# Optimization experiments

Measured on AMD Instinct MI355X. Metric: run time of the kernel, lower is better.

The kernel has to match this reference:

```python
import jax, jax.numpy as jnp
import numpy as np

D = 1024
H = 16
K = 32768
EPS = 1e-5


def setup_inputs() -> dict:
    key = jax.random.key(0)
    ks = jax.random.split(key, 12)
    s = 1.0 / np.sqrt(D)
    return {
        "query": jax.random.normal(ks[0], (D,), jnp.float32),
        "neighbors": jax.random.normal(ks[1], (K, D), jnp.float32),
        # nn.MultiheadAttention params
        "in_proj_w": jax.random.uniform(ks[2], (3 * D, D), jnp.float32, -s, s),
        "in_proj_b": jnp.zeros((3 * D,), jnp.float32),
        "out_proj_w": jax.random.uniform(ks[3], (D, D), jnp.float32, -s, s),
        "out_proj_b": jnp.zeros((D,), jnp.float32),
        # FFN params
        "w1": jax.random.uniform(ks[4], (4 * D, D), jnp.float32, -s, s),
        "b1": jnp.zeros((4 * D,), jnp.float32),
        "w2": jax.random.uniform(ks[5], (D, 4 * D), jnp.float32, -s, s),
        "b2": jnp.zeros((D,), jnp.float32),
        # LayerNorm params
        "g1": jnp.ones((D,), jnp.float32),
        "be1": jnp.zeros((D,), jnp.float32),
        "g2": jnp.ones((D,), jnp.float32),
        "be2": jnp.zeros((D,), jnp.float32),
    }


def _layernorm(x, g, b):
    m = jnp.mean(x, axis=-1, keepdims=True)
    v = jnp.var(x, axis=-1, keepdims=True)
    return (x - m) * jax.lax.rsqrt(v + EPS) * g + b


def reference(query, neighbors, in_proj_w, in_proj_b, out_proj_w, out_proj_b,
              w1, b1, w2, b2, g1, be1, g2, be2):
    dh = D // H
    wq, wk, wv = in_proj_w[:D], in_proj_w[D:2 * D], in_proj_w[2 * D:]
    bq, bk, bv = in_proj_b[:D], in_proj_b[D:2 * D], in_proj_b[2 * D:]

    q = (query @ wq.T + bq).reshape(H, dh)            # [H, dh]
    k = (neighbors @ wk.T + bk).reshape(K, H, dh)     # [K, H, dh]
    v = (neighbors @ wv.T + bv).reshape(K, H, dh)

    scores = jnp.einsum('hd,khd->hk', q, k) / np.sqrt(dh)  # [H, K]
    attn = jax.nn.softmax(scores, axis=-1)
    ctx = jnp.einsum('hk,khd->hd', attn, v).reshape(D)      # [D]
    attn_out = ctx @ out_proj_w.T + out_proj_b

    x = _layernorm(query + attn_out, g1, be1)
    ffn = jax.nn.gelu(x @ w1.T + b1, approximate=False) @ w2.T + b2
    return _layernorm(x + ffn, g2, be2)
```

## Files before the change

### kernel.cpp

```cpp
#include <hip/hip_runtime.h>
#include <hip/hip_bf16.h>

#define D 1024
#define H 16
#define DH 64
#define KN 32768
#define EPS 1e-5f

__device__ __forceinline__ float wave_sum(float v){
  #pragma unroll
  for (int off = 32; off; off >>= 1) v += __shfl_xor(v, off, 64);
  return v;
}

#define GLL(gp, lp) __builtin_amdgcn_global_load_lds((const __attribute__((address_space(1))) void*)(gp), (__attribute__((address_space(3))) void*)(lp), 16, 0, 0)

__global__ void g_qproj(const float* __restrict__ query, const float* __restrict__ ipw,
                        const float* __restrict__ ipb, float* __restrict__ q){
  int j = blockIdx.x, l = threadIdx.x;
  const float4* qv = (const float4*)(query + l*16);
  const float4* wv = (const float4*)(ipw + (size_t)j*D + l*16);
  float acc = 0.f;
  #pragma unroll
  for (int t = 0; t < 4; t++){
    float4 a = qv[t], b = wv[t];
    acc += a.x*b.x + a.y*b.y + a.z*b.z + a.w*b.w;
  }
  acc = wave_sum(acc);
  if (l == 0) q[j] = acc + ipb[j];
}

__global__ __launch_bounds__(256) void g_qk(const float* __restrict__ ipw, const float* __restrict__ ipb,
                                            const float* __restrict__ q, float* __restrict__ qk,
                                            float* __restrict__ sb){
  int b = blockIdx.x, t = threadIdx.x;
  int h = b >> 2, sl = b & 3;
  int jg = t >> 6, c = t & 63;
  __shared__ float qh[DH];
  __shared__ float4 red[256];
  if (t < DH) qh[t] = q[h*DH + t];
  __syncthreads();
  if (t < DH){
    float p = qh[t] * ipb[D + h*DH + t];
    p = wave_sum(p);
    if (t == 0 && sl == 0) sb[h] = p;
  }
  float4 acc = make_float4(0.f,0.f,0.f,0.f);
  for (int jj = 0; jj < 16; jj++){
    int j = jg*16 + jj;
    float4 w = *((const float4*)(ipw + (size_t)(D + h*DH + j)*D) + sl*64 + c);
    float qj = qh[j];
    acc.x += qj*w.x; acc.y += qj*w.y; acc.z += qj*w.z; acc.w += qj*w.w;
  }
  red[t] = acc;
  __syncthreads();
  if (jg == 0){
    float4 a = red[c], b1 = red[64+c], c1 = red[128+c], d1 = red[192+c];
    float4 r = make_float4(a.x+b1.x+c1.x+d1.x, a.y+b1.y+c1.y+d1.y,
                           a.z+b1.z+c1.z+d1.z, a.w+b1.w+c1.w+d1.w);
    ((float4*)(qk + h*D))[sl*64 + c] = r;
  }
}

__global__ void g_attn(const float* __restrict__ nbr, const float* __restrict__ qk,
                       const float* __restrict__ sb, float* __restrict__ lpart,
                       float* __restrict__ part, int rows_per_blk){
  __shared__ __align__(16) float tile[2][8*D];
  int t = threadIdx.x;
  int h = t >> 6, ci = t & 63;
  int wb = t & ~63;
  float sbh = sb[h];

  float qkv[16];
  {
    const float4* qp = (const float4*)(qk + h*D);
    #pragma unroll
    for (int c = 0; c < 4; c++){
      float4 f = qp[c*64 + ci];
      qkv[4*c]=f.x; qkv[4*c+1]=f.y; qkv[4*c+2]=f.z; qkv[4*c+3]=f.w;
    }
  }
  float acc[16];
  #pragma unroll
  for (int i = 0; i < 16; i++) acc[i] = 0.f;
  float lsum = 0.f;

  const int k0 = blockIdx.x * rows_per_blk;
  const int ntiles = rows_per_blk >> 3;
  const uint4* gb = (const uint4*)nbr;

  {
    const uint4* g = gb + (size_t)k0*256;
    #pragma unroll
    for (int i = 0; i < 2; i++) GLL(g + i*1024 + t, &tile[0][(i*1024 + wb)*4]);
  }
  __syncthreads();

  #pragma unroll 1
  for (int tl = 0; tl < ntiles; tl++){
    int cur = tl & 1;
    if (tl + 1 < ntiles){
      const uint4* g = gb + (size_t)(k0 + (tl+1)*8)*256;
      #pragma unroll
      for (int i = 0; i < 2; i++) GLL(g + i*1024 + t, &tile[cur^1][(i*1024 + wb)*4]);
    }
    #pragma unroll 1
    for (int r = 0; r < 8; r++){
      const float4* row4 = (const float4*)(tile[cur]) + r*256;
      float xf[16];
      float s = 0.f;
      #pragma unroll
      for (int c = 0; c < 4; c++){
        float4 a = row4[c*64 + ci];
        xf[4*c]=a.x; xf[4*c+1]=a.y; xf[4*c+2]=a.z; xf[4*c+3]=a.w;
        s += a.x*qkv[4*c] + a.y*qkv[4*c+1] + a.z*qkv[4*c+2] + a.w*qkv[4*c+3];
      }
      s = wave_sum(s);
      float p = __expf((s + sbh)*0.125f);
      lsum += p;
      #pragma unroll
      for (int i = 0; i < 16; i++) acc[i] += p*xf[i];
    }
    __syncthreads();
  }

  if (ci == 0) lpart[blockIdx.x*H + h] = lsum;
  float4* o = (float4*)(part + (size_t)blockIdx.x*(H*D) + h*D);
  #pragma unroll
  for (int c = 0; c < 4; c++)
    o[c*64 + ci] = make_float4(acc[4*c], acc[4*c+1], acc[4*c+2], acc[4*c+3]);
}

__global__ __launch_bounds__(256) void g_red(const float* __restrict__ part, const float* __restrict__ lpart,
                                             float* __restrict__ nb, float* __restrict__ lh, int nblk){
  int b = blockIdx.x, t = threadIdx.x;
  if (b == 64){
    if (t < H){
      float s = 0.f;
      for (int c = 0; c < nblk; c++) s += lpart[c*H + t];
      lh[t] = s;
    }
    return;
  }
  int o = b*256 + t;
  float s = 0.f;
  #pragma unroll 8
  for (int c = 0; c < nblk; c++) s += part[(size_t)c*(H*D) + o];
  nb[o] = s;
}

__global__ void g_ctx(const float* __restrict__ ipw, const float* __restrict__ ipb,
                      const float* __restrict__ nb, const float* __restrict__ lh,
                      float* __restrict__ ctx){
  int j = blockIdx.x, l = threadIdx.x, h = j >> 6;
  const float4* wv = (const float4*)(ipw + (size_t)(2*D + j)*D + l*16);
  const float4* nv = (const float4*)(nb + h*D + l*16);
  float acc = 0.f;
  #pragma unroll
  for (int t = 0; t < 4; t++){
    float4 b = wv[t], n = nv[t];
    acc += b.x*n.x + b.y*n.y + b.z*n.z + b.w*n.w;
  }
  acc = wave_sum(acc);
  if (l == 0) ctx[j] = acc/lh[h] + ipb[2*D + j];
}

__global__ void g_attnout(const float* __restrict__ opw, const float* __restrict__ opb,
                          const float* __restrict__ query, const float* __restrict__ ctx,
                          float* __restrict__ xb){
  int j = blockIdx.x, l = threadIdx.x;
  const float4* wv = (const float4*)(opw + (size_t)j*D + l*16);
  const float4* cv = (const float4*)(ctx + l*16);
  float acc = 0.f;
  #pragma unroll
  for (int t = 0; t < 4; t++){
    float4 b = wv[t], c = cv[t];
    acc += b.x*c.x + b.y*c.y + b.z*c.z + b.w*c.w;
  }
  acc = wave_sum(acc);
  if (l == 0) xb[j] = query[j] + acc + opb[j];
}

__global__ __launch_bounds__(256) void g_ffn1(const float* __restrict__ w1, const float* __restrict__ b1,
                                              const float* __restrict__ xb,
                                              const float* __restrict__ g1, const float* __restrict__ be1,
                                              float* __restrict__ xln, float* __restrict__ h1){
  int t = threadIdx.x, b = blockIdx.x;
  __shared__ float xs[D];
  __shared__ float red[8];
  float4 v = ((const float4*)xb)[t];
  float s = wave_sum(v.x + v.y + v.z + v.w);
  if ((t & 63) == 0) red[t >> 6] = s;
  __syncthreads();
  float m = (red[0]+red[1]+red[2]+red[3]) * (1.0f/D);
  float4 d = make_float4(v.x-m, v.y-m, v.z-m, v.w-m);
  float s2 = wave_sum(d.x*d.x + d.y*d.y + d.z*d.z + d.w*d.w);
  if ((t & 63) == 0) red[4 + (t >> 6)] = s2;
  __syncthreads();
  float var = (red[4]+red[5]+red[6]+red[7]) * (1.0f/D);
  float rs = rsqrtf(var + EPS);
  float4 gg = ((const float4*)g1)[t], bb = ((const float4*)be1)[t];
  float4 r = make_float4(d.x*rs*gg.x + bb.x, d.y*rs*gg.y + bb.y,
                         d.z*rs*gg.z + bb.z, d.w*rs*gg.w + bb.w);
  ((float4*)xs)[t] = r;
  if (b == 0) ((float4*)xln)[t] = r;
  __syncthreads();

  int w = t >> 6, l = t & 63;
  const float4* xs4 = (const float4*)xs;
  #pragma unroll 1
  for (int rr = 0; rr < 4; rr++){
    int j = b*16 + w*4 + rr;
    const float4* wr = (const float4*)(w1 + (size_t)j*D);
    float a = 0.f;
    #pragma unroll
    for (int c = 0; c < 4; c++){
      float4 ww = wr[c*64 + l], xx = xs4[c*64 + l];
      a += ww.x*xx.x + ww.y*xx.y + ww.z*xx.z + ww.w*xx.w;
    }
    a = wave_sum(a);
    if (l == 0){
      float z = a + b1[j];
      h1[j] = 0.5f*z*(1.0f + erff(z*0.70710678118654752f));
    }
  }
}

__global__ void g_ffn2(const float* __restrict__ w2, const float* __restrict__ b2v,
                       const float* __restrict__ h1, float* __restrict__ y){
  int j = blockIdx.x, l = threadIdx.x;
  const float4* wv = (const float4*)(w2 + (size_t)j*4096 + l*64);
  const float4* hv = (const float4*)(h1 + l*64);
  float acc = 0.f;
  #pragma unroll
  for (int t = 0; t < 16; t++){
    float4 b = wv[t], hh = hv[t];
    acc += b.x*hh.x + b.y*hh.y + b.z*hh.z + b.w*hh.w;
  }
  acc = wave_sum(acc);
  if (l == 0) y[j] = acc + b2v[j];
}

__global__ __launch_bounds__(1024) void g_ln2(const float* __restrict__ xln, const float* __restrict__ y,
                                              const float* __restrict__ g, const float* __restrict__ be,
                                              float* __restrict__ out){
  int t = threadIdx.x;
  __shared__ float red[16];
  __shared__ float bc;
  float v = xln[t] + y[t];
  float s = wave_sum(v);
  if ((t & 63) == 0) red[t >> 6] = s;
  __syncthreads();
  if (t == 0){ float a = 0.f; for (int i = 0; i < 16; i++) a += red[i]; bc = a*(1.0f/D); }
  __syncthreads();
  float m = bc;
  float d = v - m;
  float s2 = wave_sum(d*d);
  if ((t & 63) == 0) red[t >> 6] = s2;
  __syncthreads();
  if (t == 0){ float a = 0.f; for (int i = 0; i < 16; i++) a += red[i]; bc = a*(1.0f/D); }
  __syncthreads();
  float rs = rsqrtf(bc + EPS);
  out[t] = d*rs*g[t] + be[t];
}

extern "C" void kernel_launch(void* const* d_in, const int* in_sizes, int n_in,
                              void* d_out, int out_size, void* d_ws, size_t ws_size,
                              hipStream_t stream) {
  const float* query = (const float*)d_in[0];
  const float* nbr   = (const float*)d_in[1];
  const float* ipw   = (const float*)d_in[2];
  const float* ipb   = (const float*)d_in[3];
  const float* opw   = (const float*)d_in[4];
  const float* opb   = (const float*)d_in[5];
  const float* w1    = (const float*)d_in[6];
  const float* b1    = (const float*)d_in[7];
  const float* w2    = (const float*)d_in[8];
  const float* b2v   = (const float*)d_in[9];
  const float* g1    = (const float*)d_in[10];
  const float* be1   = (const float*)d_in[11];
  const float* g2    = (const float*)d_in[12];
  const float* be2   = (const float*)d_in[13];

  float* ws    = (float*)d_ws;
  float* q     = ws;
  float* qk    = q + D;
  float* sb    = qk + H*D;
  float* lh    = sb + 16;
  float* ctx   = lh + 16;
  float* xb    = ctx + D;
  float* xln   = xb + D;
  float* h1    = xln + D;
  float* y     = h1 + 4*D;
  float* nb    = y + D;
  float* lpart = nb + H*D;
  float* part  = lpart + 4096;

  size_t fixed_bytes = (size_t)(part - ws) * 4;
  int nblk = 256;
  while (nblk > 32 && fixed_bytes + (size_t)nblk*H*D*4 > ws_size) nblk >>= 1;
  int rows_per_blk = KN / nblk;

  g_qproj  <<<1024, 64, 0, stream>>>(query, ipw, ipb, q);
  g_qk     <<<64, 256, 0, stream>>>(ipw, ipb, q, qk, sb);
  g_attn   <<<nblk, 1024, 0, stream>>>(nbr, qk, sb, lpart, part, rows_per_blk);
  g_red    <<<65, 256, 0, stream>>>(part, lpart, nb, lh, nblk);
  g_ctx    <<<1024, 64, 0, stream>>>(ipw, ipb, nb, lh, ctx);
  g_attnout<<<1024, 64, 0, stream>>>(opw, opb, query, ctx, xb);
  g_ffn1   <<<256, 256, 0, stream>>>(w1, b1, xb, g1, be1, xln, h1);
  g_ffn2   <<<1024, 64, 0, stream>>>(w2, b2v, h1, y);
  g_ln2    <<<1, 1024, 0, stream>>>(xln, y, g2, be2, (float*)d_out);
}
```

Baseline: 347.3 us.

## Process four heads per wave in attention kernel with 256-thread blocks

The attention kernel now runs 256 threads per block, and each wave handles four heads instead of one. It computes four partial dot products and merges them with a shared butterfly reduction, broadcasting the four probabilities for the weighted accumulation. This cuts the number of waves that read each neighbor tile from LDS and raises the block count to 512 with two blocks per CU. The reduction kernel is reworked to split the block dimension across four thread groups, combined through shared memory. In exchange, each thread holds far more registers, and the partial buffer becomes larger to reduce.

```diff
diff --git a/kernel.cpp b/kernel.cpp
--- a/kernel.cpp
+++ b/kernel.cpp
@@ -62,27 +62,34 @@
   }
 }
 
-__global__ void g_attn(const float* __restrict__ nbr, const float* __restrict__ qk,
+__global__ __launch_bounds__(256, 2) void g_attn(const float* __restrict__ nbr, const float* __restrict__ qk,
                        const float* __restrict__ sb, float* __restrict__ lpart,
                        float* __restrict__ part, int rows_per_blk){
   __shared__ __align__(16) float tile[2][8*D];
-  int t = threadIdx.x;
-  int h = t >> 6, ci = t & 63;
-  int wb = t & ~63;
-  float sbh = sb[h];
-
-  float qkv[16];
+  const int t = threadIdx.x;
+  const int w = t >> 6, ci = t & 63;
+  const int wb = t & ~63;
+  const int g = (ci >> 4) & 3;
+  const float sbl = sb[w*4 + g];
+
+  float qk0[16], qk1[16], qk2[16], qk3[16];
   {
-    const float4* qp = (const float4*)(qk + h*D);
+    const float4* p0 = (const float4*)(qk + (w*4+0)*D);
+    const float4* p1 = (const float4*)(qk + (w*4+1)*D);
+    const float4* p2 = (const float4*)(qk + (w*4+2)*D);
+    const float4* p3 = (const float4*)(qk + (w*4+3)*D);
     #pragma unroll
     for (int c = 0; c < 4; c++){
-      float4 f = qp[c*64 + ci];
-      qkv[4*c]=f.x; qkv[4*c+1]=f.y; qkv[4*c+2]=f.z; qkv[4*c+3]=f.w;
-    }
-  }
-  float acc[16];
-  #pragma unroll
-  for (int i = 0; i < 16; i++) acc[i] = 0.f;
+      float4 f;
+      f = p0[c*64 + ci]; qk0[4*c]=f.x; qk0[4*c+1]=f.y; qk0[4*c+2]=f.z; qk0[4*c+3]=f.w;
+      f = p1[c*64 + ci]; qk1[4*c]=f.x; qk1[4*c+1]=f.y; qk1[4*c+2]=f.z; qk1[4*c+3]=f.w;
+      f = p2[c*64 + ci]; qk2[4*c]=f.x; qk2[4*c+1]=f.y; qk2[4*c+2]=f.z; qk2[4*c+3]=f.w;
+      f = p3[c*64 + ci]; qk3[4*c]=f.x; qk3[4*c+1]=f.y; qk3[4*c+2]=f.z; qk3[4*c+3]=f.w;
+    }
+  }
+  float acc0[16], acc1[16], acc2[16], acc3[16];
+  #pragma unroll
+  for (int i = 0; i < 16; i++){ acc0[i]=0.f; acc1[i]=0.f; acc2[i]=0.f; acc3[i]=0.f; }
   float lsum = 0.f;
 
   const int k0 = blockIdx.x * rows_per_blk;
@@ -90,9 +97,9 @@
   const uint4* gb = (const uint4*)nbr;
 
   {
-    const uint4* g = gb + (size_t)k0*256;
+    const uint4* gsrc = gb + (size_t)k0*256;
     #pragma unroll
-    for (int i = 0; i < 2; i++) GLL(g + i*1024 + t, &tile[0][(i*1024 + wb)*4]);
+    for (int i = 0; i < 8; i++) GLL(gsrc + i*256 + t, &tile[0][(i*256 + wb)*4]);
   }
   __syncthreads();
 
@@ -100,53 +107,95 @@
   for (int tl = 0; tl < ntiles; tl++){
     int cur = tl & 1;
     if (tl + 1 < ntiles){
-      const uint4* g = gb + (size_t)(k0 + (tl+1)*8)*256;
+      const uint4* gsrc = gb + (size_t)(k0 + (tl+1)*8)*256;
       #pragma unroll
-      for (int i = 0; i < 2; i++) GLL(g + i*1024 + t, &tile[cur^1][(i*1024 + wb)*4]);
+      for (int i = 0; i < 8; i++) GLL(gsrc + i*256 + t, &tile[cur^1][(i*256 + wb)*4]);
     }
     #pragma unroll 1
     for (int r = 0; r < 8; r++){
       const float4* row4 = (const float4*)(tile[cur]) + r*256;
       float xf[16];
-      float s = 0.f;
+      float s0=0.f, s1=0.f, s2=0.f, s3=0.f;
       #pragma unroll
       for (int c = 0; c < 4; c++){
         float4 a = row4[c*64 + ci];
         xf[4*c]=a.x; xf[4*c+1]=a.y; xf[4*c+2]=a.z; xf[4*c+3]=a.w;
-        s += a.x*qkv[4*c] + a.y*qkv[4*c+1] + a.z*qkv[4*c+2] + a.w*qkv[4*c+3];
+        s0 += a.x*qk0[4*c] + a.y*qk0[4*c+1] + a.z*qk0[4*c+2] + a.w*qk0[4*c+3];
+        s1 += a.x*qk1[4*c] + a.y*qk1[4*c+1] + a.z*qk1[4*c+2] + a.w*qk1[4*c+3];
+        s2 += a.x*qk2[4*c] + a.y*qk2[4*c+1] + a.z*qk2[4*c+2] + a.w*qk2[4*c+3];
+        s3 += a.x*qk3[4*c] + a.y*qk3[4*c+1] + a.z*qk3[4*c+2] + a.w*qk3[4*c+3];
       }
-      s = wave_sum(s);
-      float p = __expf((s + sbh)*0.125f);
-      lsum += p;
+      const bool lo32 = (ci & 32) == 0;
+      float za = lo32 ? s2 : s0;
+      float ka = lo32 ? s0 : s2;
+      float u02 = ka + __shfl_xor(za, 32, 64);
+      float zb = lo32 ? s3 : s1;
+      float kb = lo32 ? s1 : s3;
+      float u13 = kb + __shfl_xor(zb, 32, 64);
+      const bool lo16 = (ci & 16) == 0;
+      float zc = lo16 ? u13 : u02;
+      float kc = lo16 ? u02 : u13;
+      float v = kc + __shfl_xor(zc, 16, 64);
+      v += __shfl_xor(v, 8, 64);
+      v += __shfl_xor(v, 4, 64);
+      v += __shfl_xor(v, 2, 64);
+      v += __shfl_xor(v, 1, 64);
+      float pv = __expf((v + sbl)*0.125f);
+      lsum += pv;
+      float p0 = __shfl(pv, 0, 64);
+      float p1 = __shfl(pv, 16, 64);
+      float p2 = __shfl(pv, 32, 64);
+      float p3 = __shfl(pv, 48, 64);
       #pragma unroll
-      for (int i = 0; i < 16; i++) acc[i] += p*xf[i];
+      for (int j = 0; j < 16; j++){
+        acc0[j] += p0*xf[j];
+        acc1[j] += p1*xf[j];
+        acc2[j] += p2*xf[j];
+        acc3[j] += p3*xf[j];
+      }
     }
     __syncthreads();
   }
 
-  if (ci == 0) lpart[blockIdx.x*H + h] = lsum;
-  float4* o = (float4*)(part + (size_t)blockIdx.x*(H*D) + h*D);
-  #pragma unroll
-  for (int c = 0; c < 4; c++)
-    o[c*64 + ci] = make_float4(acc[4*c], acc[4*c+1], acc[4*c+2], acc[4*c+3]);
+  if ((ci & 15) == 0) lpart[blockIdx.x*H + w*4 + g] = lsum;
+  float4* o = (float4*)(part + (size_t)blockIdx.x*(H*D) + (size_t)(w*4)*D);
+  #pragma unroll
+  for (int c = 0; c < 4; c++){
+    o[0*256 + c*64 + ci] = make_float4(acc0[4*c], acc0[4*c+1], acc0[4*c+2], acc0[4*c+3]);
+    o[1*256 + c*64 + ci] = make_float4(acc1[4*c], acc1[4*c+1], acc1[4*c+2], acc1[4*c+3]);
+    o[2*256 + c*64 + ci] = make_float4(acc2[4*c], acc2[4*c+1], acc2[4*c+2], acc2[4*c+3]);
+    o[3*256 + c*64 + ci] = make_float4(acc3[4*c], acc3[4*c+1], acc3[4*c+2], acc3[4*c+3]);
+  }
 }
 
 __global__ __launch_bounds__(256) void g_red(const float* __restrict__ part, const float* __restrict__ lpart,
                                              float* __restrict__ nb, float* __restrict__ lh, int nblk){
   int b = blockIdx.x, t = threadIdx.x;
-  if (b == 64){
-    if (t < H){
-      float s = 0.f;
-      for (int c = 0; c < nblk; c++) s += lpart[c*H + t];
-      lh[t] = s;
+  __shared__ float red[256];
+  if (b == 256){
+    int h = t & 15, cs = t >> 4;
+    int per = nblk >> 4;
+    float s = 0.f;
+    for (int k = 0; k < per; k++) s += lpart[(cs*per + k)*H + h];
+    red[t] = s;
+    __syncthreads();
+    if (t < 16){
+      float a = 0.f;
+      #pragma unroll
+      for (int i = 0; i < 16; i++) a += red[i*16 + t];
+      lh[t] = a;
     }
     return;
   }
-  int o = b*256 + t;
+  int o0 = b * 64;
+  int oo = t & 63, cs = t >> 6;
+  int per = nblk >> 2;
   float s = 0.f;
   #pragma unroll 8
-  for (int c = 0; c < nblk; c++) s += part[(size_t)c*(H*D) + o];
-  nb[o] = s;
+  for (int k = 0; k < per; k++) s += part[(size_t)(cs*per + k)*(H*D) + o0 + oo];
+  red[t] = s;
+  __syncthreads();
+  if (t < 64) nb[o0 + t] = red[t] + red[64+t] + red[128+t] + red[192+t];
 }
 
 __global__ void g_ctx(const float* __restrict__ ipw, const float* __restrict__ ipb,
@@ -294,17 +343,17 @@
   float* y     = h1 + 4*D;
   float* nb    = y + D;
   float* lpart = nb + H*D;
-  float* part  = lpart + 4096;
+  float* part  = lpart + 8192;
 
   size_t fixed_bytes = (size_t)(part - ws) * 4;
-  int nblk = 256;
-  while (nblk > 32 && fixed_bytes + (size_t)nblk*H*D*4 > ws_size) nblk >>= 1;
+  int nblk = 512;
+  while (nblk > 64 && fixed_bytes + (size_t)nblk*H*D*4 > ws_size) nblk >>= 1;
   int rows_per_blk = KN / nblk;
 
   g_qproj  <<<1024, 64, 0, stream>>>(query, ipw, ipb, q);
   g_qk     <<<64, 256, 0, stream>>>(ipw, ipb, q, qk, sb);
-  g_attn   <<<nblk, 1024, 0, stream>>>(nbr, qk, sb, lpart, part, rows_per_blk);
-  g_red    <<<65, 256, 0, stream>>>(part, lpart, nb, lh, nblk);
+  g_attn   <<<nblk, 256, 0, stream>>>(nbr, qk, sb, lpart, part, rows_per_blk);
+  g_red    <<<257, 256, 0, stream>>>(part, lpart, nb, lh, nblk);
   g_ctx    <<<1024, 64, 0, stream>>>(ipw, ipb, nb, lh, ctx);
   g_attnout<<<1024, 64, 0, stream>>>(opw, opb, query, ctx, xb);
   g_ffn1   <<<256, 256, 0, stream>>>(w1, b1, xb, g1, be1, xln, h1);
```

Measured after the change: 299.4 us. -13.8%, faster.
